# Optimization experiments

Hardware: AMD Instinct MI355X
Metric: run time of the kernel (lower is better)

## Reference

```python
import jax, jax.numpy as jnp
import numpy as np

N, T, C_IN, H, C_OUT = 50000, 8, 32, 128, 32
E = 800000


def setup_inputs() -> dict:
    key = jax.random.key(0)
    ks = jax.random.split(key, 16)
    s = 0.05
    return {
        "x": jax.random.normal(ks[0], (N, T, C_IN), dtype=jnp.float32),
        "edge_index": jax.random.randint(ks[1], (2, E), 0, N, dtype=jnp.int64),
        # SAGEConv: lin_l applied to mean-aggregated neighbors (with bias), lin_r to root (no bias)
        "Wl": jax.random.normal(ks[2], (H, C_IN), dtype=jnp.float32) * s,
        "bl": jnp.zeros((H,), dtype=jnp.float32),
        "Wr": jax.random.normal(ks[3], (H, C_IN), dtype=jnp.float32) * s,
        # GRU (torch layout: gates stacked [r; z; n])
        "W_ih": jax.random.normal(ks[4], (3 * H, H), dtype=jnp.float32) * s,
        "b_ih": jnp.zeros((3 * H,), dtype=jnp.float32),
        "W_hh": jax.random.normal(ks[5], (3 * H, H), dtype=jnp.float32) * s,
        "b_hh": jnp.zeros((3 * H,), dtype=jnp.float32),
        # heads
        "W_rec": jax.random.normal(ks[6], (C_OUT, H), dtype=jnp.float32) * s,
        "b_rec": jnp.zeros((C_OUT,), dtype=jnp.float32),
        "W_c1": jax.random.normal(ks[7], (H // 2, H), dtype=jnp.float32) * s,
        "b_c1": jnp.zeros((H // 2,), dtype=jnp.float32),
        "W_c2": jax.random.normal(ks[8], (1, H // 2), dtype=jnp.float32) * s,
        "b_c2": jnp.zeros((1,), dtype=jnp.float32),
    }


def _st_graph_sage(x, edge_index, Wl, bl, Wr, W_ih, b_ih, W_hh, b_hh,
                   W_rec, b_rec, W_c1, b_c1, W_c2, b_c2):
    n_nodes = x.shape[0]
    src, dst = edge_index[0], edge_index[1]
    # in-degree for mean aggregation (avoid div-by-zero for isolated nodes)
    deg = jax.ops.segment_sum(jnp.ones_like(dst, dtype=x.dtype), dst,
                              num_segments=n_nodes)
    deg = jnp.maximum(deg, 1.0)[:, None]
    hdim = W_hh.shape[1]

    def step(h, x_t):
        # SAGEConv (mean aggr): lin_l(mean_j x_j) + lin_r(x_i)
        agg = jax.ops.segment_sum(x_t[src], dst, num_segments=n_nodes) / deg
        sp = jax.nn.relu(agg @ Wl.T + bl + x_t @ Wr.T)
        # single-step GRU (torch equations)
        gx = sp @ W_ih.T + b_ih
        gh = h @ W_hh.T + b_hh
        gx_r, gx_z, gx_n = jnp.split(gx, 3, axis=-1)
        gh_r, gh_z, gh_n = jnp.split(gh, 3, axis=-1)
        r = jax.nn.sigmoid(gx_r + gh_r)
        z = jax.nn.sigmoid(gx_z + gh_z)
        n = jnp.tanh(gx_n + r * gh_n)
        h_new = (1.0 - z) * n + z * h
        return h_new, h_new

    h0 = jnp.zeros((n_nodes, hdim), dtype=x.dtype)
    _, hs = jax.lax.scan(step, h0, jnp.transpose(x, (1, 0, 2)))  # hs: [T, N, H]

    recon = hs @ W_rec.T + b_rec                                  # [T, N, C_OUT]
    cls = jax.nn.sigmoid(jax.nn.relu(hs @ W_c1.T + b_c1) @ W_c2.T + b_c2)  # [T, N, 1]
    reconstruction_output = jnp.transpose(recon, (1, 0, 2))       # [N, T, C_OUT]
    classification_output = jnp.transpose(cls[..., 0], (1, 0))    # [N, T]
    return reconstruction_output, classification_output


def reference(x, edge_index, Wl, bl, Wr, W_ih, b_ih, W_hh, b_hh,
              W_rec, b_rec, W_c1, b_c1, W_c2, b_c2):
    return _st_graph_sage(x, edge_index, Wl, bl, Wr, W_ih, b_ih, W_hh, b_hh,
                          W_rec, b_rec, W_c1, b_c1, W_c2, b_c2)
```

## Files before the change

### kernel.cpp

```cpp
#include <hip/hip_runtime.h>
#include <hip/hip_bf16.h>

#define N_NODES 50000
#define T_STEPS 8
#define CIN     32
#define HDIM    128
#define E_EDGES 800000
#define NBLK    196

typedef __attribute__((ext_vector_type(8))) short  short8;
typedef __attribute__((ext_vector_type(4))) float  f32x4;

__device__ __forceinline__ ushort f2b(float f) {
    __hip_bfloat16 b = __float2bfloat16(f);
    return *reinterpret_cast<ushort*>(&b);
}
__device__ __forceinline__ float b2f(ushort u) { return __uint_as_float(((uint)u) << 16); }
__device__ __forceinline__ float sigm(float x)  { return 1.f / (1.f + __expf(-x)); }
__device__ __forceinline__ float tanhx(float x) { float e = __expf(2.f * x); return 1.f - 2.f / (e + 1.f); }
__device__ __forceinline__ int SW(int fl) { return fl ^ (fl >> 3); }

__global__ void k_deg(const int* __restrict__ ei, int* __restrict__ deg) {
    int e = blockIdx.x * 256 + threadIdx.x;
    if (e < E_EDGES) atomicAdd(&deg[ei[E_EDGES + e]], 1);
}

__global__ __launch_bounds__(256)
void k_scan1(const int* __restrict__ deg, int* __restrict__ incl, int* __restrict__ bsum) {
    __shared__ int sA[256], sB[256];
    int tid = threadIdx.x;
    int i = blockIdx.x * 256 + tid;
    sA[tid] = (i < N_NODES) ? deg[i] : 0;
    __syncthreads();
    int* rd = sA; int* wr = sB;
    for (int off = 1; off < 256; off <<= 1) {
        int v = rd[tid];
        if (tid >= off) v += rd[tid - off];
        wr[tid] = v;
        __syncthreads();
        int* tmp = rd; rd = wr; wr = tmp;
    }
    incl[i] = rd[tid];
    if (tid == 255) bsum[blockIdx.x] = rd[255];
}

__global__ void k_scan2(const int* __restrict__ bsum, int* __restrict__ boff,
                        int* __restrict__ row_ptr) {
    __shared__ int sA[256], sB[256];
    int tid = threadIdx.x;
    int v0 = (tid < NBLK) ? bsum[tid] : 0;
    sA[tid] = v0;
    __syncthreads();
    int* rd = sA; int* wr = sB;
    for (int off = 1; off < 256; off <<= 1) {
        int v = rd[tid];
        if (tid >= off) v += rd[tid - off];
        wr[tid] = v;
        __syncthreads();
        int* tmp = rd; rd = wr; wr = tmp;
    }
    if (tid < NBLK) boff[tid] = rd[tid] - v0;
    if (tid == NBLK - 1) row_ptr[N_NODES] = rd[tid];
}

__global__ __launch_bounds__(256)
void k_scan3(const int* __restrict__ deg, const int* __restrict__ incl,
             const int* __restrict__ boff, int* __restrict__ row_ptr,
             int* __restrict__ cursor, float* __restrict__ rdeg) {
    int i = blockIdx.x * 256 + threadIdx.x;
    if (i >= N_NODES) return;
    int d = deg[i];
    int excl = incl[i] - d + boff[blockIdx.x];
    row_ptr[i] = excl;
    cursor[i]  = excl;
    rdeg[i] = 1.0f / (float)max(d, 1);
}

__global__ void k_bucket(const int* __restrict__ ei, int* __restrict__ cursor,
                         int* __restrict__ csr_src) {
    int e = blockIdx.x * 256 + threadIdx.x;
    if (e < E_EDGES) {
        int d = ei[E_EDGES + e];
        int slot = atomicAdd(&cursor[d], 1);
        csr_src[slot] = ei[e];
    }
}

__global__ __launch_bounds__(256)
void k_xbf(const float* __restrict__ x, ushort* __restrict__ xb) {
    size_t i = ((size_t)blockIdx.x * 256 + threadIdx.x) * 4;
    float4 v = *(const float4*)(x + i);
    ushort4 o; o.x = f2b(v.x); o.y = f2b(v.y); o.z = f2b(v.z); o.w = f2b(v.w);
    *(ushort4*)(xb + i) = o;
}

__global__ void k_pack(const float* __restrict__ Wih, const float* __restrict__ Whh,
                       const float* __restrict__ Wl,  const float* __restrict__ Wr,
                       const float* __restrict__ Wrec,const float* __restrict__ Wc1,
                       short* __restrict__ Bf, short* __restrict__ Bsf, short* __restrict__ B2f) {
    int i = blockIdx.x * 256 + threadIdx.x;
    if (i < 131072) {
        int b = i & 7, lane = (i >> 3) & 63, ks = (i >> 9) & 7, ct = i >> 12;
        int col = ct * 16 + (lane & 15);
        int k = ks * 32 + ((lane >> 4) << 3) + b;
        float v;
        if (col < 256)      v = (k < 128) ? Wih[col * 128 + k] : Whh[col * 128 + (k - 128)];
        else if (col < 384) v = (k < 128) ? Wih[col * 128 + k] : 0.f;
        else                v = (k >= 128) ? Whh[(col - 128) * 128 + (k - 128)] : 0.f;
        Bf[i] = (short)f2b(v);
    } else if (i < 139264) {
        int t2 = i - 131072;
        int b = t2 & 7, lane = (t2 >> 3) & 63, ks = (t2 >> 9) & 1, ct = t2 >> 10;
        int col = ct * 16 + (lane & 15);
        int k = ks * 32 + ((lane >> 4) << 3) + b;
        float v = (k < 32) ? Wl[col * 32 + k] : Wr[col * 32 + (k - 32)];
        Bsf[t2] = (short)f2b(v);
    } else if (i < 151552) {
        int t3 = i - 139264;
        int b = t3 & 7, lane = (t3 >> 3) & 63, ks = (t3 >> 9) & 3, ct = t3 >> 11;
        int col = ct * 16 + (lane & 15);
        int k = ks * 32 + ((lane >> 4) << 3) + b;
        float v = (col < 32) ? Wrec[col * 128 + k] : Wc1[(col - 32) * 128 + k];
        B2f[t3] = (short)f2b(v);
    }
}

__global__ __launch_bounds__(256)
void k_agg_all(const ushort* __restrict__ xb, const int* __restrict__ row_ptr,
               const int* __restrict__ csr_src, const float* __restrict__ rdeg,
               ushort* __restrict__ aggb) {
    int g = blockIdx.x * 256 + threadIdx.x;
    int node = g >> 3, st = (g & 7) * 4;
    if (node >= N_NODES) return;
    int e0 = row_ptr[node], e1 = row_ptr[node + 1];
    float acc[8][4];
#pragma unroll
    for (int t = 0; t < 8; ++t)
#pragma unroll
        for (int c = 0; c < 4; ++c) acc[t][c] = 0.f;
    for (int e = e0; e < e1; ++e) {
        int s = csr_src[e];
        const ushort* b = xb + (size_t)s * (T_STEPS * CIN) + st;
#pragma unroll
        for (int t = 0; t < 8; ++t) {
            ushort4 v = *(const ushort4*)(b + t * CIN);
            acc[t][0] += b2f(v.x); acc[t][1] += b2f(v.y);
            acc[t][2] += b2f(v.z); acc[t][3] += b2f(v.w);
        }
    }
    float r = rdeg[node];
    ushort* o = aggb + (size_t)node * (T_STEPS * CIN) + st;
#pragma unroll
    for (int t = 0; t < 8; ++t) {
        ushort4 v; v.x = f2b(acc[t][0] * r); v.y = f2b(acc[t][1] * r);
        v.z = f2b(acc[t][2] * r); v.w = f2b(acc[t][3] * r);
        *(ushort4*)(o + t * CIN) = v;
    }
}

__global__ __launch_bounds__(512, 2)
void k_rec(const ushort* __restrict__ aggb, const ushort* __restrict__ xb,
           const short* __restrict__ Bsf, const short* __restrict__ Bf,
           const short* __restrict__ B2f,
           const float* __restrict__ bl,
           const float* __restrict__ b_ih, const float* __restrict__ b_hh,
           const float* __restrict__ b_rec, const float* __restrict__ b_c1,
           const float* __restrict__ W_c2, const float* __restrict__ b_c2,
           float* __restrict__ out_rec, float* __restrict__ out_cls) {
    __shared__ short lds[20480];
    const int tid = threadIdx.x;
    const int nb  = blockIdx.x * 64;
    const int wv   = __builtin_amdgcn_readfirstlane(tid >> 6);
    const int lane = tid & 63;
    const int li   = lane & 15, lq = lane >> 4;
    const int j    = wv * 16 + li;

    for (int c = tid; c < 1024; c += 512)
        *(short8*)&lds[8192 + c * 8] = (short8){0, 0, 0, 0, 0, 0, 0, 0};

    float hold[4][4];
#pragma unroll
    for (int ri = 0; ri < 4; ++ri)
#pragma unroll
        for (int q = 0; q < 4; ++q) hold[ri][q] = 0.f;

    const float blc  = bl[j];
    const float br_  = b_ih[j]       + b_hh[j];
    const float bz_  = b_ih[128 + j] + b_hh[128 + j];
    const float bihn = b_ih[256 + j], bhhn = b_hh[256 + j];

    const int snode = tid >> 3, sk0 = (tid & 7) * 8;
    const int sgn = nb + snode;
    const ushort* sp0 = nullptr;
    if (sgn < N_NODES)
        sp0 = ((sk0 < 32) ? aggb : xb) + (size_t)sgn * (T_STEPS * CIN) + (sk0 & 31);
    const int sdst = 16384 + (((sk0 >> 5) * 4 + (snode >> 4)) * 64
                              + SW(((sk0 & 31) >> 3) * 16 + (snode & 15))) * 8;
    short8 pv = (short8){0, 0, 0, 0, 0, 0, 0, 0};
    if (sp0) pv = *(const short8*)(sp0);

    for (int t = 0; t < T_STEPS; ++t) {
        *(short8*)&lds[sdst] = pv;
        __syncthreads();
        if (sp0 && t + 1 < T_STEPS) pv = *(const short8*)(sp0 + (t + 1) * CIN);

        {
            f32x4 accS[4];
#pragma unroll
            for (int ri = 0; ri < 4; ++ri) accS[ri] = (f32x4){0.f, 0.f, 0.f, 0.f};
#pragma unroll
            for (int ks = 0; ks < 2; ++ks) {
                short8 a[4];
#pragma unroll
                for (int ri = 0; ri < 4; ++ri)
                    a[ri] = *(short8*)&lds[16384 + ((ks * 4 + ri) * 64 + SW(lane)) * 8];
                short8 b = *(const short8*)(Bsf + ((wv * 2 + ks) * 64 + lane) * 8);
#pragma unroll
                for (int ri = 0; ri < 4; ++ri)
                    accS[ri] = __builtin_amdgcn_mfma_f32_16x16x32_bf16(a[ri], b, accS[ri], 0, 0, 0);
            }
            int ks_t = j >> 5, lh = (j & 31) >> 3, jj = j & 7;
#pragma unroll
            for (int ri = 0; ri < 4; ++ri)
#pragma unroll
                for (int q = 0; q < 4; ++q) {
                    float v = fmaxf(accS[ri][q] + blc, 0.f);
                    lds[((ks_t * 4 + ri) * 64 + SW(lh * 16 + lq * 4 + q)) * 8 + jj] = (short)f2b(v);
                }
        }
        __syncthreads();

        f32x4 acc[4][4];
#pragma unroll
        for (int g = 0; g < 4; ++g)
#pragma unroll
            for (int ri = 0; ri < 4; ++ri) acc[g][ri] = (f32x4){0.f, 0.f, 0.f, 0.f};
#pragma unroll 2
        for (int ks = 0; ks < 8; ++ks) {
            short8 av[4];
#pragma unroll
            for (int ri = 0; ri < 4; ++ri)
                av[ri] = *(short8*)&lds[((ks * 4 + ri) * 64 + SW(lane)) * 8];
            short8 bv[4];
#pragma unroll
            for (int g = 0; g < 4; ++g)
                bv[g] = *(const short8*)(Bf + (((g * 8 + wv) * 8 + ks) * 64 + lane) * 8);
#pragma unroll
            for (int g = 0; g < 4; ++g)
#pragma unroll
                for (int ri = 0; ri < 4; ++ri)
                    acc[g][ri] = __builtin_amdgcn_mfma_f32_16x16x32_bf16(av[ri], bv[g], acc[g][ri], 0, 0, 0);
        }

#pragma unroll
        for (int ri = 0; ri < 4; ++ri)
#pragma unroll
            for (int q = 0; q < 4; ++q) {
                float r = sigm(acc[0][ri][q] + br_);
                float z = sigm(acc[1][ri][q] + bz_);
                float nn = tanhx(acc[2][ri][q] + bihn + r * (acc[3][ri][q] + bhhn));
                hold[ri][q] = (1.f - z) * nn + z * hold[ri][q];
            }
        __syncthreads();

        {
            int ks_h = 4 + (j >> 5), lh_h = (j & 31) >> 3, jj_h = j & 7;
#pragma unroll
            for (int ri = 0; ri < 4; ++ri)
#pragma unroll
                for (int q = 0; q < 4; ++q)
                    lds[((ks_h * 4 + ri) * 64 + SW(lh_h * 16 + lq * 4 + q)) * 8 + jj_h]
                        = (short)f2b(hold[ri][q]);
        }
        __syncthreads();

        float* c1f = (float*)lds;
        if (wv < 6) {
            f32x4 accH[4];
#pragma unroll
            for (int ri = 0; ri < 4; ++ri) accH[ri] = (f32x4){0.f, 0.f, 0.f, 0.f};
#pragma unroll
            for (int ksh = 0; ksh < 4; ++ksh) {
                short8 a[4];
#pragma unroll
                for (int ri = 0; ri < 4; ++ri)
                    a[ri] = *(short8*)&lds[(((4 + ksh) * 4 + ri) * 64 + SW(lane)) * 8];
                short8 b = *(const short8*)(B2f + ((wv * 4 + ksh) * 64 + lane) * 8);
#pragma unroll
                for (int ri = 0; ri < 4; ++ri)
                    accH[ri] = __builtin_amdgcn_mfma_f32_16x16x32_bf16(a[ri], b, accH[ri], 0, 0, 0);
            }
            int col = wv * 16 + li;
            if (col < 32) {
                float br = b_rec[col];
#pragma unroll
                for (int ri = 0; ri < 4; ++ri)
#pragma unroll
                    for (int q = 0; q < 4; ++q) {
                        int row = ri * 16 + lq * 4 + q, gn = nb + row;
                        if (gn < N_NODES)
                            out_rec[(size_t)gn * (T_STEPS * 32) + t * 32 + col] = accH[ri][q] + br;
                    }
            } else {
                int cc = col - 32;
                float bc = b_c1[cc];
#pragma unroll
                for (int ri = 0; ri < 4; ++ri)
#pragma unroll
                    for (int q = 0; q < 4; ++q) {
                        int row = ri * 16 + lq * 4 + q;
                        c1f[row * 64 + (cc ^ (row & 31))] = fmaxf(accH[ri][q] + bc, 0.f);
                    }
            }
        }
        __syncthreads();

        {
            int node = tid >> 3, st = tid & 7, gn = nb + node;
            float s = 0.f;
#pragma unroll
            for (int c = 0; c < 8; ++c) {
                int q = st * 8 + c;
                s = fmaf(W_c2[q], c1f[node * 64 + (q ^ (node & 31))], s);
            }
            s += __shfl_xor(s, 1);
            s += __shfl_xor(s, 2);
            s += __shfl_xor(s, 4);
            if (st == 0 && gn < N_NODES)
                out_cls[(size_t)gn * T_STEPS + t] = sigm(s + b_c2[0]);
        }
    }
}

extern "C" void kernel_launch(void* const* d_in, const int* in_sizes, int n_in,
                              void* d_out, int out_size, void* d_ws, size_t ws_size,
                              hipStream_t stream) {
    const float* x     = (const float*)d_in[0];
    const int*   ei    = (const int*)  d_in[1];
    const float* Wl    = (const float*)d_in[2];
    const float* bl    = (const float*)d_in[3];
    const float* Wr    = (const float*)d_in[4];
    const float* W_ih  = (const float*)d_in[5];
    const float* b_ih  = (const float*)d_in[6];
    const float* W_hh  = (const float*)d_in[7];
    const float* b_hh  = (const float*)d_in[8];
    const float* W_rec = (const float*)d_in[9];
    const float* b_rec = (const float*)d_in[10];
    const float* W_c1  = (const float*)d_in[11];
    const float* b_c1  = (const float*)d_in[12];
    const float* W_c2  = (const float*)d_in[13];
    const float* b_c2  = (const float*)d_in[14];

    char* wp = (char*)d_ws;
    auto alloc = [&](size_t bytes) -> char* {
        char* p = wp; wp += (bytes + 255) & ~(size_t)255; return p;
    };
    int*    deg     = (int*)   alloc((size_t)N_NODES * 4);
    int*    row_ptr = (int*)   alloc((size_t)(N_NODES + 1) * 4);
    int*    cursor  = (int*)   alloc((size_t)N_NODES * 4);
    int*    csr_src = (int*)   alloc((size_t)E_EDGES * 4);
    float*  rdeg    = (float*) alloc((size_t)N_NODES * 4);
    int*    incl    = (int*)   alloc((size_t)NBLK * 256 * 4);
    int*    bsum    = (int*)   alloc((size_t)256 * 4);
    int*    boff    = (int*)   alloc((size_t)256 * 4);
    short*  Bf      = (short*) alloc((size_t)131072 * 2);
    short*  Bsf     = (short*) alloc((size_t)8192 * 2);
    short*  B2f     = (short*) alloc((size_t)12288 * 2);
    ushort* xb      = (ushort*)alloc((size_t)N_NODES * T_STEPS * CIN * 2);
    ushort* aggb    = (ushort*)alloc((size_t)N_NODES * T_STEPS * CIN * 2);

    float* out_rec = (float*)d_out;
    float* out_cls = out_rec + (size_t)N_NODES * T_STEPS * 32;

    hipMemsetAsync(deg, 0, (size_t)N_NODES * 4, stream);

    k_deg   <<<(E_EDGES + 255) / 256, 256, 0, stream>>>(ei, deg);
    k_scan1 <<<NBLK, 256, 0, stream>>>(deg, incl, bsum);
    k_scan2 <<<1, 256, 0, stream>>>(bsum, boff, row_ptr);
    k_scan3 <<<NBLK, 256, 0, stream>>>(deg, incl, boff, row_ptr, cursor, rdeg);
    k_bucket<<<(E_EDGES + 255) / 256, 256, 0, stream>>>(ei, cursor, csr_src);
    k_xbf   <<<12500, 256, 0, stream>>>(x, xb);
    k_pack  <<<592, 256, 0, stream>>>(W_ih, W_hh, Wl, Wr, W_rec, W_c1, Bf, Bsf, B2f);

    k_agg_all<<<(N_NODES * 8 + 255) / 256, 256, 0, stream>>>(
        xb, row_ptr, csr_src, rdeg, aggb);
    k_rec<<<(N_NODES + 63) / 64, 512, 0, stream>>>(
        aggb, xb, Bsf, Bf, B2f, bl, b_ih, b_hh, b_rec, b_c1, W_c2, b_c2,
        out_rec, out_cls);
}
```

Baseline: 485.1 us.

## Skip zero blocks in GRU n-gate MFMA and defer head computation one step

The packed GRU weight matrix no longer stores the zero halves of the n-gate columns, so each wave does 12 MFMA chains per k-step instead of 16. The output heads (reconstruction and classifier) for step t-1 now run inside step t, overlapped with the SAGE stage and the GRU epilogue. This removes two block-wide barriers per timestep, with c1f moved to its own LDS region so it is not overwritten. Launch bounds are raised to ask for 4 waves per SIMD, which may force register spills given the larger live state.

Result: slower. 610.8 us (+25.9%).

```diff
diff --git a/kernel.cpp b/kernel.cpp
--- a/kernel.cpp
+++ b/kernel.cpp
@@ -99,24 +99,33 @@
                        const float* __restrict__ Wrec,const float* __restrict__ Wc1,
                        short* __restrict__ Bf, short* __restrict__ Bsf, short* __restrict__ B2f) {
     int i = blockIdx.x * 256 + threadIdx.x;
-    if (i < 131072) {
+    if (i < 65536) {
         int b = i & 7, lane = (i >> 3) & 63, ks = (i >> 9) & 7, ct = i >> 12;
         int col = ct * 16 + (lane & 15);
         int k = ks * 32 + ((lane >> 4) << 3) + b;
-        float v;
-        if (col < 256)      v = (k < 128) ? Wih[col * 128 + k] : Whh[col * 128 + (k - 128)];
-        else if (col < 384) v = (k < 128) ? Wih[col * 128 + k] : 0.f;
-        else                v = (k >= 128) ? Whh[(col - 128) * 128 + (k - 128)] : 0.f;
+        float v = (k < 128) ? Wih[col * 128 + k] : Whh[col * 128 + (k - 128)];
         Bf[i] = (short)f2b(v);
-    } else if (i < 139264) {
-        int t2 = i - 131072;
+    } else if (i < 81920) {
+        int t2 = i - 65536;
+        int b = t2 & 7, lane = (t2 >> 3) & 63, ks = (t2 >> 9) & 3, ct = t2 >> 11;
+        int col = 256 + ct * 16 + (lane & 15);
+        int k = ks * 32 + ((lane >> 4) << 3) + b;
+        Bf[i] = (short)f2b(Wih[col * 128 + k]);
+    } else if (i < 98304) {
+        int t2 = i - 81920;
+        int b = t2 & 7, lane = (t2 >> 3) & 63, ks = (t2 >> 9) & 3, ct = t2 >> 11;
+        int col = 256 + ct * 16 + (lane & 15);
+        int k = ks * 32 + ((lane >> 4) << 3) + b;
+        Bf[i] = (short)f2b(Whh[col * 128 + k]);
+    } else if (i < 106496) {
+        int t2 = i - 98304;
         int b = t2 & 7, lane = (t2 >> 3) & 63, ks = (t2 >> 9) & 1, ct = t2 >> 10;
         int col = ct * 16 + (lane & 15);
         int k = ks * 32 + ((lane >> 4) << 3) + b;
         float v = (k < 32) ? Wl[col * 32 + k] : Wr[col * 32 + (k - 32)];
         Bsf[t2] = (short)f2b(v);
-    } else if (i < 151552) {
-        int t3 = i - 139264;
+    } else if (i < 118784) {
+        int t3 = i - 106496;
         int b = t3 & 7, lane = (t3 >> 3) & 63, ks = (t3 >> 9) & 3, ct = t3 >> 11;
         int col = ct * 16 + (lane & 15);
         int k = ks * 32 + ((lane >> 4) << 3) + b;
@@ -158,7 +167,7 @@
     }
 }
 
-__global__ __launch_bounds__(512, 2)
+__global__ __launch_bounds__(512, 4)
 void k_rec(const ushort* __restrict__ aggb, const ushort* __restrict__ xb,
            const short* __restrict__ Bsf, const short* __restrict__ Bf,
            const short* __restrict__ B2f,
@@ -167,7 +176,8 @@
            const float* __restrict__ b_rec, const float* __restrict__ b_c1,
            const float* __restrict__ W_c2, const float* __restrict__ b_c2,
            float* __restrict__ out_rec, float* __restrict__ out_cls) {
-    __shared__ short lds[20480];
+    __shared__ short lds[28672];
+    float* c1f = (float*)&lds[20480];
     const int tid = threadIdx.x;
     const int nb  = blockIdx.x * 64;
     const int wv   = __builtin_amdgcn_readfirstlane(tid >> 6);
@@ -188,6 +198,9 @@
     const float br_  = b_ih[j]       + b_hh[j];
     const float bz_  = b_ih[128 + j] + b_hh[128 + j];
     const float bihn = b_ih[256 + j], bhhn = b_hh[256 + j];
+    float bhead = 0.f;
+    if (wv < 2)      bhead = b_rec[j];
+    else if (wv < 6) bhead = b_c1[j - 32];
 
     const int snode = tid >> 3, sk0 = (tid & 7) * 8;
     const int sgn = nb + snode;
@@ -199,6 +212,56 @@
     short8 pv = (short8){0, 0, 0, 0, 0, 0, 0, 0};
     if (sp0) pv = *(const short8*)(sp0);
 
+    auto do_heads = [&](int tt) {
+        f32x4 accH[4];
+#pragma unroll
+        for (int ri = 0; ri < 4; ++ri) accH[ri] = (f32x4){0.f, 0.f, 0.f, 0.f};
+#pragma unroll
+        for (int ksh = 0; ksh < 4; ++ksh) {
+            short8 a[4];
+#pragma unroll
+            for (int ri = 0; ri < 4; ++ri)
+                a[ri] = *(short8*)&lds[(((4 + ksh) * 4 + ri) * 64 + SW(lane)) * 8];
+            short8 b = *(const short8*)(B2f + ((wv * 4 + ksh) * 64 + lane) * 8);
+#pragma unroll
+            for (int ri = 0; ri < 4; ++ri)
+                accH[ri] = __builtin_amdgcn_mfma_f32_16x16x32_bf16(a[ri], b, accH[ri], 0, 0, 0);
+        }
+        if (wv < 2) {
+#pragma unroll
+            for (int ri = 0; ri < 4; ++ri)
+#pragma unroll
+                for (int q = 0; q < 4; ++q) {
+                    int row = ri * 16 + lq * 4 + q, gn = nb + row;
+                    if (gn < N_NODES)
+                        out_rec[(size_t)gn * (T_STEPS * 32) + tt * 32 + j] = accH[ri][q] + bhead;
+                }
+        } else {
+            int cc = j - 32;
+#pragma unroll
+            for (int ri = 0; ri < 4; ++ri)
+#pragma unroll
+                for (int q = 0; q < 4; ++q) {
+                    int row = ri * 16 + lq * 4 + q;
+                    c1f[row * 64 + (cc ^ (row & 31))] = fmaxf(accH[ri][q] + bhead, 0.f);
+                }
+        }
+    };
+    auto do_cls = [&](int tt) {
+        int node = tid >> 3, st = tid & 7, gn2 = nb + node;
+        float s = 0.f;
+#pragma unroll
+        for (int c = 0; c < 8; ++c) {
+            int q = st * 8 + c;
+            s = fmaf(W_c2[q], c1f[node * 64 + (q ^ (node & 31))], s);
+        }
+        s += __shfl_xor(s, 1);
+        s += __shfl_xor(s, 2);
+        s += __shfl_xor(s, 4);
+        if (st == 0 && gn2 < N_NODES)
+            out_cls[(size_t)gn2 * T_STEPS + tt] = sigm(s + b_c2[0]);
+    };
+
     for (int t = 0; t < T_STEPS; ++t) {
         *(short8*)&lds[sdst] = pv;
         __syncthreads();
@@ -219,6 +282,7 @@
                 for (int ri = 0; ri < 4; ++ri)
                     accS[ri] = __builtin_amdgcn_mfma_f32_16x16x32_bf16(a[ri], b, accS[ri], 0, 0, 0);
             }
+            if (t > 0 && wv < 6) do_heads(t - 1);
             int ks_t = j >> 5, lh = (j & 31) >> 3, jj = j & 7;
 #pragma unroll
             for (int ri = 0; ri < 4; ++ri)
@@ -230,37 +294,57 @@
         }
         __syncthreads();
 
-        f32x4 acc[4][4];
-#pragma unroll
-        for (int g = 0; g < 4; ++g)
-#pragma unroll
-            for (int ri = 0; ri < 4; ++ri) acc[g][ri] = (f32x4){0.f, 0.f, 0.f, 0.f};
-#pragma unroll 2
-        for (int ks = 0; ks < 8; ++ks) {
+        f32x4 accRZ[2][4], accN1[4], accN2[4];
+#pragma unroll
+        for (int ri = 0; ri < 4; ++ri) {
+            accRZ[0][ri] = (f32x4){0.f, 0.f, 0.f, 0.f};
+            accRZ[1][ri] = (f32x4){0.f, 0.f, 0.f, 0.f};
+            accN1[ri]    = (f32x4){0.f, 0.f, 0.f, 0.f};
+            accN2[ri]    = (f32x4){0.f, 0.f, 0.f, 0.f};
+        }
+#pragma unroll
+        for (int ks = 0; ks < 4; ++ks) {
             short8 av[4];
 #pragma unroll
             for (int ri = 0; ri < 4; ++ri)
                 av[ri] = *(short8*)&lds[((ks * 4 + ri) * 64 + SW(lane)) * 8];
-            short8 bv[4];
-#pragma unroll
-            for (int g = 0; g < 4; ++g)
-                bv[g] = *(const short8*)(Bf + (((g * 8 + wv) * 8 + ks) * 64 + lane) * 8);
-#pragma unroll
-            for (int g = 0; g < 4; ++g)
-#pragma unroll
-                for (int ri = 0; ri < 4; ++ri)
-                    acc[g][ri] = __builtin_amdgcn_mfma_f32_16x16x32_bf16(av[ri], bv[g], acc[g][ri], 0, 0, 0);
+            short8 b0 = *(const short8*)(Bf + (((0 * 8 + wv) * 8 + ks) * 64 + lane) * 8);
+            short8 b1 = *(const short8*)(Bf + (((1 * 8 + wv) * 8 + ks) * 64 + lane) * 8);
+            short8 bn = *(const short8*)(Bf + (65536 + ((wv * 4 + ks) * 64 + lane) * 8));
+#pragma unroll
+            for (int ri = 0; ri < 4; ++ri) {
+                accRZ[0][ri] = __builtin_amdgcn_mfma_f32_16x16x32_bf16(av[ri], b0, accRZ[0][ri], 0, 0, 0);
+                accRZ[1][ri] = __builtin_amdgcn_mfma_f32_16x16x32_bf16(av[ri], b1, accRZ[1][ri], 0, 0, 0);
+                accN1[ri]    = __builtin_amdgcn_mfma_f32_16x16x32_bf16(av[ri], bn, accN1[ri], 0, 0, 0);
+            }
+        }
+#pragma unroll
+        for (int ks = 4; ks < 8; ++ks) {
+            short8 av[4];
+#pragma unroll
+            for (int ri = 0; ri < 4; ++ri)
+                av[ri] = *(short8*)&lds[((ks * 4 + ri) * 64 + SW(lane)) * 8];
+            short8 b0 = *(const short8*)(Bf + (((0 * 8 + wv) * 8 + ks) * 64 + lane) * 8);
+            short8 b1 = *(const short8*)(Bf + (((1 * 8 + wv) * 8 + ks) * 64 + lane) * 8);
+            short8 bn = *(const short8*)(Bf + (81920 + ((wv * 4 + (ks - 4)) * 64 + lane) * 8));
+#pragma unroll
+            for (int ri = 0; ri < 4; ++ri) {
+                accRZ[0][ri] = __builtin_amdgcn_mfma_f32_16x16x32_bf16(av[ri], b0, accRZ[0][ri], 0, 0, 0);
+                accRZ[1][ri] = __builtin_amdgcn_mfma_f32_16x16x32_bf16(av[ri], b1, accRZ[1][ri], 0, 0, 0);
+                accN2[ri]    = __builtin_amdgcn_mfma_f32_16x16x32_bf16(av[ri], bn, accN2[ri], 0, 0, 0);
+            }
         }
 
 #pragma unroll
         for (int ri = 0; ri < 4; ++ri)
 #pragma unroll
             for (int q = 0; q < 4; ++q) {
-                float r = sigm(acc[0][ri][q] + br_);
-                float z = sigm(acc[1][ri][q] + bz_);
-                float nn = tanhx(acc[2][ri][q] + bihn + r * (acc[3][ri][q] + bhhn));
+                float r = sigm(accRZ[0][ri][q] + br_);
+                float z = sigm(accRZ[1][ri][q] + bz_);
+                float nn = tanhx(accN1[ri][q] + bihn + r * (accN2[ri][q] + bhhn));
                 hold[ri][q] = (1.f - z) * nn + z * hold[ri][q];
             }
+        if (t > 0) do_cls(t - 1);
         __syncthreads();
 
         {
@@ -272,64 +356,12 @@
                     lds[((ks_h * 4 + ri) * 64 + SW(lh_h * 16 + lq * 4 + q)) * 8 + jj_h]
                         = (short)f2b(hold[ri][q]);
         }
-        __syncthreads();
-
-        float* c1f = (float*)lds;
-        if (wv < 6) {
-            f32x4 accH[4];
-#pragma unroll
-            for (int ri = 0; ri < 4; ++ri) accH[ri] = (f32x4){0.f, 0.f, 0.f, 0.f};
-#pragma unroll
-            for (int ksh = 0; ksh < 4; ++ksh) {
-                short8 a[4];
-#pragma unroll
-                for (int ri = 0; ri < 4; ++ri)
-                    a[ri] = *(short8*)&lds[(((4 + ksh) * 4 + ri) * 64 + SW(lane)) * 8];
-                short8 b = *(const short8*)(B2f + ((wv * 4 + ksh) * 64 + lane) * 8);
-#pragma unroll
-                for (int ri = 0; ri < 4; ++ri)
-                    accH[ri] = __builtin_amdgcn_mfma_f32_16x16x32_bf16(a[ri], b, accH[ri], 0, 0, 0);
-            }
-            int col = wv * 16 + li;
-            if (col < 32) {
-                float br = b_rec[col];
-#pragma unroll
-                for (int ri = 0; ri < 4; ++ri)
-#pragma unroll
-                    for (int q = 0; q < 4; ++q) {
-                        int row = ri * 16 + lq * 4 + q, gn = nb + row;
-                        if (gn < N_NODES)
-                            out_rec[(size_t)gn * (T_STEPS * 32) + t * 32 + col] = accH[ri][q] + br;
-                    }
-            } else {
-                int cc = col - 32;
-                float bc = b_c1[cc];
-#pragma unroll
-                for (int ri = 0; ri < 4; ++ri)
-#pragma unroll
-                    for (int q = 0; q < 4; ++q) {
-                        int row = ri * 16 + lq * 4 + q;
-                        c1f[row * 64 + (cc ^ (row & 31))] = fmaxf(accH[ri][q] + bc, 0.f);
-                    }
-            }
-        }
-        __syncthreads();
-
-        {
-            int node = tid >> 3, st = tid & 7, gn = nb + node;
-            float s = 0.f;
-#pragma unroll
-            for (int c = 0; c < 8; ++c) {
-                int q = st * 8 + c;
-                s = fmaf(W_c2[q], c1f[node * 64 + (q ^ (node & 31))], s);
-            }
-            s += __shfl_xor(s, 1);
-            s += __shfl_xor(s, 2);
-            s += __shfl_xor(s, 4);
-            if (st == 0 && gn < N_NODES)
-                out_cls[(size_t)gn * T_STEPS + t] = sigm(s + b_c2[0]);
-        }
-    }
+    }
+
+    __syncthreads();
+    if (wv < 6) do_heads(T_STEPS - 1);
+    __syncthreads();
+    do_cls(T_STEPS - 1);
 }
 
 extern "C" void kernel_launch(void* const* d_in, const int* in_sizes, int n_in,
@@ -363,7 +395,7 @@
     int*    incl    = (int*)   alloc((size_t)NBLK * 256 * 4);
     int*    bsum    = (int*)   alloc((size_t)256 * 4);
     int*    boff    = (int*)   alloc((size_t)256 * 4);
-    short*  Bf      = (short*) alloc((size_t)131072 * 2);
+    short*  Bf      = (short*) alloc((size_t)98304 * 2);
     short*  Bsf     = (short*) alloc((size_t)8192 * 2);
     short*  B2f     = (short*) alloc((size_t)12288 * 2);
     ushort* xb      = (ushort*)alloc((size_t)N_NODES * T_STEPS * CIN * 2);
@@ -380,7 +412,7 @@
     k_scan3 <<<NBLK, 256, 0, stream>>>(deg, incl, boff, row_ptr, cursor, rdeg);
     k_bucket<<<(E_EDGES + 255) / 256, 256, 0, stream>>>(ei, cursor, csr_src);
     k_xbf   <<<12500, 256, 0, stream>>>(x, xb);
-    k_pack  <<<592, 256, 0, stream>>>(W_ih, W_hh, Wl, Wr, W_rec, W_c1, Bf, Bsf, B2f);
+    k_pack  <<<464, 256, 0, stream>>>(W_ih, W_hh, Wl, Wr, W_rec, W_c1, Bf, Bsf, B2f);
 
     k_agg_all<<<(N_NODES * 8 + 255) / 256, 256, 0, stream>>>(
         xb, row_ptr, csr_src, rdeg, aggb);
```
